# Kernel optimization log

Hardware: AMD Instinct MI355X
Metric: run time of the kernel (lower is better)

The kernel has to match this reference:

```python
import jax, jax.numpy as jnp
import numpy as np

DECAY = 0.99
EPS = 1e-05


def setup_inputs() -> dict:
    key = jax.random.key(0)
    k1, k2, k3 = jax.random.split(key, 3)
    return {
        "input": jax.random.normal(k1, (32, 64, 64, 64), dtype=jnp.float32),
        "embed": jax.random.normal(k2, (64, 512), dtype=jnp.float32),
        "cluster_size": jnp.zeros((512,), dtype=jnp.float32),
        "embed_avg": jax.random.normal(k3, (64, 512), dtype=jnp.float32),
    }


def reference(input, embed, cluster_size, embed_avg):
    n_embed = embed.shape[1]
    flatten = input.reshape(-1, input.shape[-1])  # [N, dim]
    dist = (
        jnp.sum(flatten * flatten, axis=1, keepdims=True)
        - 2.0 * flatten @ embed
        + jnp.sum(embed * embed, axis=0, keepdims=True)
    )  # [N, n_embed]
    embed_ind_flat = jnp.argmin(dist, axis=1)  # [N]
    embed_ind = embed_ind_flat.reshape(input.shape[:-1])
    quantize = jnp.take(embed.T, embed_ind_flat, axis=0).reshape(input.shape)
    diff = jnp.mean((quantize - input) ** 2)

    # EMA codebook update (training path; buffer updates returned as outputs)
    embed_onehot_sum = jnp.zeros((n_embed,), dtype=flatten.dtype).at[embed_ind_flat].add(1.0)
    embed_sum = jax.ops.segment_sum(flatten, embed_ind_flat, num_segments=n_embed).T  # [dim, n_embed]
    new_cluster_size = cluster_size * DECAY + (1.0 - DECAY) * embed_onehot_sum
    new_embed_avg = embed_avg * DECAY + (1.0 - DECAY) * embed_sum
    n = jnp.sum(new_cluster_size)
    cs = (new_cluster_size + EPS) / (n + n_embed * EPS) * n
    new_embed = new_embed_avg / cs[None, :]

    # straight-through estimator
    quantize_st = input + jax.lax.stop_gradient(quantize - input)
    return (quantize_st, diff, embed_ind, new_embed, new_cluster_size, new_embed_avg)
```

## Files before the change

kernel.cpp:

```cpp
#include <hip/hip_runtime.h>

#define DIM     64
#define N_EMBED 512
#define N_ROWS  131072
#define XPAD    132

__global__ void prep_kernel(const float* __restrict__ embed,
                            float* __restrict__ se,
                            float* __restrict__ embed_t,
                            int do_et) {
    int j = blockIdx.x * blockDim.x + threadIdx.x;
    if (j >= N_EMBED) return;
    float s = 0.f;
#pragma unroll
    for (int d = 0; d < DIM; d += 4) {
        float b0 = embed[(d + 0) * N_EMBED + j];
        float b1 = embed[(d + 1) * N_EMBED + j];
        float b2 = embed[(d + 2) * N_EMBED + j];
        float b3 = embed[(d + 3) * N_EMBED + j];
        s = fmaf(b0, b0, s); s = fmaf(b1, b1, s);
        s = fmaf(b2, b2, s); s = fmaf(b3, b3, s);
        if (do_et) {
            float4 v; v.x = b0; v.y = b1; v.z = b2; v.w = b3;
            *reinterpret_cast<float4*>(&embed_t[j * DIM + d]) = v;
        }
    }
    se[j] = s;
}

__launch_bounds__(256, 2)
__global__ void vq_assign(const float* __restrict__ input,
                          const float* __restrict__ embed,
                          const float* __restrict__ se,
                          float* __restrict__ out_ind,
                          int*   __restrict__ ind) {
    __shared__ float Xs[64][XPAD];
    __shared__ float Es[64][XPAD];
    __shared__ float sxs[128];

    const int t    = threadIdx.x;
    const int row0 = blockIdx.x * 128;
    const int tr   = t >> 4;
    const int tc   = t & 15;
    const int bx   = ((tc >> 2) & 1) * 4;

#pragma unroll
    for (int ph = 0; ph < 8; ++ph) {
        int idx = ph * 256 + t;
        int row = idx >> 4;
        int kq  = idx & 15;
        float4 v = *reinterpret_cast<const float4*>(
            &input[(size_t)(row0 + row) * 64 + kq * 4]);
        Xs[kq * 4 + 0][row] = v.x;
        Xs[kq * 4 + 1][row] = v.y;
        Xs[kq * 4 + 2][row] = v.z;
        Xs[kq * 4 + 3][row] = v.w;
    }
    __syncthreads();

    if (t < 128) {
        float s = 0.f;
#pragma unroll 8
        for (int k = 0; k < 64; ++k) { float x = Xs[k][t]; s = fmaf(x, x, s); }
        sxs[t] = s;
    }

    float bestd[8], sx[8];
    int   bestj[8];
#pragma unroll
    for (int r = 0; r < 8; ++r) { bestd[r] = INFINITY; bestj[r] = 0; }

    for (int chunk = 0; chunk < 4; ++chunk) {
        const int ccb = chunk * 128;
        __syncthreads();
#pragma unroll
        for (int ph = 0; ph < 8; ++ph) {
            int idx = ph * 256 + t;
            int k   = idx >> 5;
            int cq  = idx & 31;
            float4 v = *reinterpret_cast<const float4*>(
                &embed[k * N_EMBED + ccb + cq * 4]);
            *reinterpret_cast<float4*>(&Es[k][(cq * 4) ^ (((cq >> 3) & 1) * 4)]) = v;
        }
        __syncthreads();
        if (chunk == 0) {
#pragma unroll
            for (int r = 0; r < 8; ++r) sx[r] = sxs[tr * 8 + r];
        }

        float acc[8][8];
#pragma unroll
        for (int r = 0; r < 8; ++r)
#pragma unroll
            for (int c = 0; c < 8; ++c) acc[r][c] = 0.f;

#pragma unroll 2
        for (int k = 0; k < 64; ++k) {
            float a[8], b[8];
            *reinterpret_cast<float4*>(&a[0]) = *reinterpret_cast<const float4*>(&Xs[k][tr * 8]);
            *reinterpret_cast<float4*>(&a[4]) = *reinterpret_cast<const float4*>(&Xs[k][tr * 8 + 4]);
            *reinterpret_cast<float4*>(&b[0]) = *reinterpret_cast<const float4*>(&Es[k][(tc * 8) ^ bx]);
            *reinterpret_cast<float4*>(&b[4]) = *reinterpret_cast<const float4*>(&Es[k][(tc * 8 + 4) ^ bx]);
#pragma unroll
            for (int r = 0; r < 8; ++r)
#pragma unroll
                for (int c = 0; c < 8; ++c)
                    acc[r][c] = fmaf(a[r], b[c], acc[r][c]);
        }

#pragma unroll
        for (int c = 0; c < 8; ++c) {
            int j = ccb + tc * 8 + c;
            float sej = se[j];
#pragma unroll
            for (int r = 0; r < 8; ++r) {
                float d = (sx[r] - 2.f * acc[r][c]) + sej;
                if (d < bestd[r]) { bestd[r] = d; bestj[r] = j; }
            }
        }
    }

    __syncthreads();
    float* rd = &Es[0][0];
    int*   rj = (int*)(rd + 128 * 17);
#pragma unroll
    for (int r = 0; r < 8; ++r) {
        rd[(tr * 8 + r) * 17 + tc] = bestd[r];
        rj[(tr * 8 + r) * 17 + tc] = bestj[r];
    }
    __syncthreads();
    if (t < 128) {
        float bd = rd[t * 17 + 0];
        int   bj = rj[t * 17 + 0];
#pragma unroll
        for (int w = 1; w < 16; ++w) {
            float dw = rd[t * 17 + w];
            int   jw = rj[t * 17 + w];
            if (dw < bd || (dw == bd && jw < bj)) { bd = dw; bj = jw; }
        }
        out_ind[row0 + t] = (float)bj;
        ind[row0 + t]     = bj;
    }
}

__launch_bounds__(512, 1)
__global__ void vq_post(const float* __restrict__ input,
                        const float* __restrict__ embed,
                        const float* __restrict__ embed_t,
                        const int* __restrict__ ind,
                        float* __restrict__ out_q,
                        float* __restrict__ esum,
                        float* __restrict__ counts,
                        double* __restrict__ diff_acc,
                        int have_et) {
    __shared__ float lesum[DIM * N_EMBED];
    __shared__ float lcount[N_EMBED];
    __shared__ float wsum[8];
    const int t = threadIdx.x;

    float4* l4 = reinterpret_cast<float4*>(lesum);
#pragma unroll
    for (int i = 0; i < 16; ++i) l4[t + i * 512] = float4{0.f, 0.f, 0.f, 0.f};
    lcount[t] = 0.f;
    __syncthreads();

    const int row = blockIdx.x * 512 + t;
    const int j = ind[row];
    atomicAdd(&lcount[j], 1.0f);
    const float* rp = input + (size_t)row * DIM;
    float* oq = out_q + (size_t)row * DIM;
    float dsum = 0.f;

    if (have_et) {
        const float* qp = embed_t + (size_t)j * DIM;
#pragma unroll
        for (int d = 0; d < DIM; d += 4) {
            float4 v = *reinterpret_cast<const float4*>(rp + d);
            float4 q = *reinterpret_cast<const float4*>(qp + d);
            float t0 = q.x - v.x, t1 = q.y - v.y, t2 = q.z - v.z, t3 = q.w - v.w;
            float4 o;
            o.x = v.x + t0; o.y = v.y + t1; o.z = v.z + t2; o.w = v.w + t3;
            *reinterpret_cast<float4*>(oq + d) = o;
            dsum = fmaf(t0, t0, dsum); dsum = fmaf(t1, t1, dsum);
            dsum = fmaf(t2, t2, dsum); dsum = fmaf(t3, t3, dsum);
            atomicAdd(&lesum[(d + 0) * N_EMBED + j], v.x);
            atomicAdd(&lesum[(d + 1) * N_EMBED + j], v.y);
            atomicAdd(&lesum[(d + 2) * N_EMBED + j], v.z);
            atomicAdd(&lesum[(d + 3) * N_EMBED + j], v.w);
        }
    } else {
#pragma unroll
        for (int d = 0; d < DIM; d += 4) {
            float4 v = *reinterpret_cast<const float4*>(rp + d);
            float q0 = embed[(d + 0) * N_EMBED + j];
            float q1 = embed[(d + 1) * N_EMBED + j];
            float q2 = embed[(d + 2) * N_EMBED + j];
            float q3 = embed[(d + 3) * N_EMBED + j];
            float t0 = q0 - v.x, t1 = q1 - v.y, t2 = q2 - v.z, t3 = q3 - v.w;
            float4 o;
            o.x = v.x + t0; o.y = v.y + t1; o.z = v.z + t2; o.w = v.w + t3;
            *reinterpret_cast<float4*>(oq + d) = o;
            dsum = fmaf(t0, t0, dsum); dsum = fmaf(t1, t1, dsum);
            dsum = fmaf(t2, t2, dsum); dsum = fmaf(t3, t3, dsum);
            atomicAdd(&lesum[(d + 0) * N_EMBED + j], v.x);
            atomicAdd(&lesum[(d + 1) * N_EMBED + j], v.y);
            atomicAdd(&lesum[(d + 2) * N_EMBED + j], v.z);
            atomicAdd(&lesum[(d + 3) * N_EMBED + j], v.w);
        }
    }
    __syncthreads();

    for (int i = t; i < DIM * N_EMBED; i += 512) {
        float v = lesum[i];
        if (v != 0.f) atomicAdd(&esum[i], v);
    }
    {
        float v = lcount[t];
        if (v != 0.f) atomicAdd(&counts[t], v);
    }

    for (int off = 32; off > 0; off >>= 1) dsum += __shfl_down(dsum, off, 64);
    int lane = t & 63, wid = t >> 6;
    if (lane == 0) wsum[wid] = dsum;
    __syncthreads();
    if (t == 0) {
        float b = 0.f;
#pragma unroll
        for (int w = 0; w < 8; ++w) b += wsum[w];
        atomicAdd(diff_acc, (double)b);
    }
}

__global__ void fin_a(const float* __restrict__ cluster_size,
                      const float* __restrict__ counts,
                      float* __restrict__ out_ncs,
                      float* __restrict__ nstore) {
    int t = threadIdx.x;
    float ncs = cluster_size[t] * 0.99f + 0.01f * counts[t];
    out_ncs[t] = ncs;
    __shared__ float red[512];
    red[t] = ncs;
    __syncthreads();
    for (int s = 256; s > 0; s >>= 1) {
        if (t < s) red[t] += red[t + s];
        __syncthreads();
    }
    if (t == 0) nstore[0] = red[0];
}

__global__ void fin_b(const float* __restrict__ embed_avg,
                      const float* __restrict__ esum,
                      const float* __restrict__ out_ncs,
                      const float* __restrict__ nstore,
                      const double* __restrict__ diff_acc,
                      float* __restrict__ out_ne,
                      float* __restrict__ out_nea,
                      float* __restrict__ out_diff) {
    int e = blockIdx.x * 512 + threadIdx.x;
    const float EPSF = 1e-5f;
    float n = nstore[0];
    int j = e & (N_EMBED - 1);
    float ncs = out_ncs[j];
    float cs = (ncs + EPSF) / (n + 512.0f * EPSF) * n;
    float es = embed_avg[e] * 0.99f + 0.01f * esum[e];
    out_nea[e] = es;
    out_ne[e] = es / cs;
    if (e == 0) out_diff[0] = (float)(*diff_acc * (1.0 / 8388608.0));
}

extern "C" void kernel_launch(void* const* d_in, const int* in_sizes, int n_in,
                              void* d_out, int out_size, void* d_ws, size_t ws_size,
                              hipStream_t stream) {
    const float* input        = (const float*)d_in[0];
    const float* embed        = (const float*)d_in[1];
    const float* cluster_size = (const float*)d_in[2];
    const float* embed_avg    = (const float*)d_in[3];

    float* out_q    = (float*)d_out;
    float* out_diff = out_q + 8388608;
    float* out_ind  = out_diff + 1;
    float* out_ne   = out_ind + 131072;
    float* out_ncs  = out_ne + 32768;
    float* out_nea  = out_ncs + 512;

    char*   ws       = (char*)d_ws;
    double* diff_acc = (double*)ws;
    float*  nstore   = (float*)(ws + 64);
    float*  counts   = (float*)(ws + 256);
    float*  se       = (float*)(ws + 4096);
    int*    ind      = (int*)(ws + 8192);
    float*  esum     = (float*)(ws + 8192 + 524288);
    float*  embed_t  = (float*)(ws + 8192 + 524288 + 131072);

    const size_t need_et = 8192 + 524288 + 131072 + 131072;
    const int have_et = (ws_size >= need_et) ? 1 : 0;

    hipMemsetAsync(ws, 0, 4096, stream);
    hipMemsetAsync(ws + 8192 + 524288, 0, 131072, stream);
    prep_kernel<<<2, 256, 0, stream>>>(embed, se, embed_t, have_et);
    vq_assign<<<1024, 256, 0, stream>>>(input, embed, se, out_ind, ind);
    vq_post<<<256, 512, 0, stream>>>(input, embed, embed_t, ind, out_q, esum, counts,
                                     diff_acc, have_et);
    fin_a<<<1, 512, 0, stream>>>(cluster_size, counts, out_ncs, nstore);
    fin_b<<<64, 512, 0, stream>>>(embed_avg, esum, out_ncs, nstore, diff_acc,
                                  out_ne, out_nea, out_diff);
}
```

Before: 280.7 us.

## Replace global atomic embed-sum with per-block partials reduced in fin_b

Adds a vq_post_p kernel that accumulates per-code input sums in shared memory and writes each block's full 64x512 partial to workspace, instead of atomically merging into a global esum. fin_b then sums the partials per element, which removes global atomic contention and the esum memset. The cost is extra workspace traffic (up to 256 partial copies of 128 KB written and read back) and a serial reduction loop in fin_b. The new path is used only when the workspace is large enough; otherwise the old path runs.

Result: slower. 312.1 us (+11.2%).

```diff
diff --git a/kernel.cpp b/kernel.cpp
--- a/kernel.cpp
+++ b/kernel.cpp
@@ -140,6 +140,73 @@
         }
         out_ind[row0 + t] = (float)bj;
         ind[row0 + t]     = bj;
+    }
+}
+
+__launch_bounds__(512, 1)
+__global__ void vq_post_p(const float* __restrict__ input,
+                          const float* __restrict__ embed_t,
+                          const int* __restrict__ ind,
+                          float* __restrict__ out_q,
+                          float* __restrict__ partials,
+                          float* __restrict__ counts,
+                          double* __restrict__ diff_acc,
+                          int niter) {
+    __shared__ float lesum[DIM * N_EMBED];
+    __shared__ float lcount[N_EMBED];
+    __shared__ float wsum[8];
+    const int t = threadIdx.x;
+
+    float4* l4 = reinterpret_cast<float4*>(lesum);
+#pragma unroll
+    for (int i = 0; i < 16; ++i) l4[t + i * 512] = float4{0.f, 0.f, 0.f, 0.f};
+    lcount[t] = 0.f;
+    __syncthreads();
+
+    float dsum = 0.f;
+    for (int it = 0; it < niter; ++it) {
+        const int row = (blockIdx.x * niter + it) * 512 + t;
+        const int j = ind[row];
+        atomicAdd(&lcount[j], 1.0f);
+        const float* rp = input + (size_t)row * DIM;
+        const float* qp = embed_t + (size_t)j * DIM;
+        float* oq = out_q + (size_t)row * DIM;
+#pragma unroll
+        for (int d = 0; d < DIM; d += 4) {
+            float4 v = *reinterpret_cast<const float4*>(rp + d);
+            float4 q = *reinterpret_cast<const float4*>(qp + d);
+            float t0 = q.x - v.x, t1 = q.y - v.y, t2 = q.z - v.z, t3 = q.w - v.w;
+            float4 o;
+            o.x = v.x + t0; o.y = v.y + t1; o.z = v.z + t2; o.w = v.w + t3;
+            *reinterpret_cast<float4*>(oq + d) = o;
+            dsum = fmaf(t0, t0, dsum); dsum = fmaf(t1, t1, dsum);
+            dsum = fmaf(t2, t2, dsum); dsum = fmaf(t3, t3, dsum);
+            atomicAdd(&lesum[(d + 0) * N_EMBED + j], v.x);
+            atomicAdd(&lesum[(d + 1) * N_EMBED + j], v.y);
+            atomicAdd(&lesum[(d + 2) * N_EMBED + j], v.z);
+            atomicAdd(&lesum[(d + 3) * N_EMBED + j], v.w);
+        }
+    }
+    __syncthreads();
+
+    float* dst = partials + (size_t)blockIdx.x * (DIM * N_EMBED);
+    for (int i = t * 4; i < DIM * N_EMBED; i += 2048) {
+        *reinterpret_cast<float4*>(dst + i) = *reinterpret_cast<float4*>(&lesum[i]);
+    }
+    {
+        float v = lcount[t];
+        if (v != 0.f) atomicAdd(&counts[t], v);
+    }
+
+    for (int off = 32; off > 0; off >>= 1) dsum += __shfl_down(dsum, off, 64);
+    int lane = t & 63, wid = t >> 6;
+    if (lane == 0) wsum[wid] = dsum;
+    __syncthreads();
+    if (t == 0) {
+        float b = 0.f;
+#pragma unroll
+        for (int w = 0; w < 8; ++w) b += wsum[w];
+        atomicAdd(diff_acc, (double)b);
     }
 }
 
@@ -249,7 +316,8 @@
 }
 
 __global__ void fin_b(const float* __restrict__ embed_avg,
-                      const float* __restrict__ esum,
+                      const float* __restrict__ src,
+                      int npart,
                       const float* __restrict__ out_ncs,
                       const float* __restrict__ nstore,
                       const double* __restrict__ diff_acc,
@@ -258,11 +326,13 @@
                       float* __restrict__ out_diff) {
     int e = blockIdx.x * 512 + threadIdx.x;
     const float EPSF = 1e-5f;
+    float s = 0.f;
+    for (int p = 0; p < npart; ++p) s += src[(size_t)p * (DIM * N_EMBED) + e];
     float n = nstore[0];
     int j = e & (N_EMBED - 1);
     float ncs = out_ncs[j];
     float cs = (ncs + EPSF) / (n + 512.0f * EPSF) * n;
-    float es = embed_avg[e] * 0.99f + 0.01f * esum[e];
+    float es = embed_avg[e] * 0.99f + 0.01f * s;
     out_nea[e] = es;
     out_ne[e] = es / cs;
     if (e == 0) out_diff[0] = (float)(*diff_acc * (1.0 / 8388608.0));
@@ -291,17 +361,33 @@
     int*    ind      = (int*)(ws + 8192);
     float*  esum     = (float*)(ws + 8192 + 524288);
     float*  embed_t  = (float*)(ws + 8192 + 524288 + 131072);
-
+    float*  partials = (float*)(ws + (1 << 20));
+
+    const size_t POFF = 1 << 20;
+    int npart = 0, niter = 0;
+    if (ws_size >= POFF + (size_t)256 * 131072)      { npart = 256; niter = 1; }
+    else if (ws_size >= POFF + (size_t)64 * 131072)  { npart = 64;  niter = 4; }
     const size_t need_et = 8192 + 524288 + 131072 + 131072;
     const int have_et = (ws_size >= need_et) ? 1 : 0;
 
     hipMemsetAsync(ws, 0, 4096, stream);
-    hipMemsetAsync(ws + 8192 + 524288, 0, 131072, stream);
-    prep_kernel<<<2, 256, 0, stream>>>(embed, se, embed_t, have_et);
-    vq_assign<<<1024, 256, 0, stream>>>(input, embed, se, out_ind, ind);
-    vq_post<<<256, 512, 0, stream>>>(input, embed, embed_t, ind, out_q, esum, counts,
-                                     diff_acc, have_et);
-    fin_a<<<1, 512, 0, stream>>>(cluster_size, counts, out_ncs, nstore);
-    fin_b<<<64, 512, 0, stream>>>(embed_avg, esum, out_ncs, nstore, diff_acc,
-                                  out_ne, out_nea, out_diff);
-}
+
+    if (npart && have_et) {
+        prep_kernel<<<2, 256, 0, stream>>>(embed, se, embed_t, 1);
+        vq_assign<<<1024, 256, 0, stream>>>(input, embed, se, out_ind, ind);
+        vq_post_p<<<npart, 512, 0, stream>>>(input, embed_t, ind, out_q, partials,
+                                             counts, diff_acc, niter);
+        fin_a<<<1, 512, 0, stream>>>(cluster_size, counts, out_ncs, nstore);
+        fin_b<<<64, 512, 0, stream>>>(embed_avg, partials, npart, out_ncs, nstore,
+                                      diff_acc, out_ne, out_nea, out_diff);
+    } else {
+        hipMemsetAsync(ws + 8192 + 524288, 0, 131072, stream);
+        prep_kernel<<<2, 256, 0, stream>>>(embed, se, embed_t, have_et);
+        vq_assign<<<1024, 256, 0, stream>>>(input, embed, se, out_ind, ind);
+        vq_post<<<256, 512, 0, stream>>>(input, embed, embed_t, ind, out_q, esum,
+                                         counts, diff_acc, have_et);
+        fin_a<<<1, 512, 0, stream>>>(cluster_size, counts, out_ncs, nstore);
+        fin_b<<<64, 512, 0, stream>>>(embed_avg, esum, 1, out_ncs, nstore,
+                                      diff_acc, out_ne, out_nea, out_diff);
+    }
+}
```

## Split post pass into quantize kernel and per-code gather segment-sum kernel

Applied to the files above, without the earlier changes.

Replaces the fused post kernel, which scattered every row into a 128KB shared histogram with LDS atomics and then flushed it to global with atomics, with two kernels. The first writes the quantized output and accumulates the squared-error sum. The second gives each code its own block: the block scans the whole index array in chunks, queues the matching rows in shared memory and sums them with coalesced per-lane loads, then writes esum and counts directly with no global atomics or memset. Each of the 512 blocks rereads the full index array and the input is gathered a second time, in exchange for removing LDS atomic contention and the single-block-per-CU occupancy limit.

Result: slower. 766.3 us (+173.0%).

```diff
diff --git a/kernel.cpp b/kernel.cpp
--- a/kernel.cpp
+++ b/kernel.cpp
@@ -4,6 +4,7 @@
 #define N_EMBED 512
 #define N_ROWS  131072
 #define XPAD    132
+#define CHUNK   4096
 
 __global__ void prep_kernel(const float* __restrict__ embed,
                             float* __restrict__ se,
@@ -143,32 +144,18 @@
     }
 }
 
-__launch_bounds__(512, 1)
-__global__ void vq_post(const float* __restrict__ input,
-                        const float* __restrict__ embed,
-                        const float* __restrict__ embed_t,
-                        const int* __restrict__ ind,
-                        float* __restrict__ out_q,
-                        float* __restrict__ esum,
-                        float* __restrict__ counts,
-                        double* __restrict__ diff_acc,
-                        int have_et) {
-    __shared__ float lesum[DIM * N_EMBED];
-    __shared__ float lcount[N_EMBED];
-    __shared__ float wsum[8];
-    const int t = threadIdx.x;
-
-    float4* l4 = reinterpret_cast<float4*>(lesum);
-#pragma unroll
-    for (int i = 0; i < 16; ++i) l4[t + i * 512] = float4{0.f, 0.f, 0.f, 0.f};
-    lcount[t] = 0.f;
-    __syncthreads();
-
-    const int row = blockIdx.x * 512 + t;
-    const int j = ind[row];
-    atomicAdd(&lcount[j], 1.0f);
-    const float* rp = input + (size_t)row * DIM;
-    float* oq = out_q + (size_t)row * DIM;
+__launch_bounds__(256)
+__global__ void vq_quant(const float* __restrict__ input,
+                         const float* __restrict__ embed,
+                         const float* __restrict__ embed_t,
+                         const int* __restrict__ ind,
+                         float* __restrict__ out_q,
+                         double* __restrict__ diff_acc,
+                         int have_et) {
+    const int i = blockIdx.x * 256 + threadIdx.x;
+    const int j = ind[i];
+    const float* rp = input + (size_t)i * DIM;
+    float* oq = out_q + (size_t)i * DIM;
     float dsum = 0.f;
 
     if (have_et) {
@@ -183,10 +170,6 @@
             *reinterpret_cast<float4*>(oq + d) = o;
             dsum = fmaf(t0, t0, dsum); dsum = fmaf(t1, t1, dsum);
             dsum = fmaf(t2, t2, dsum); dsum = fmaf(t3, t3, dsum);
-            atomicAdd(&lesum[(d + 0) * N_EMBED + j], v.x);
-            atomicAdd(&lesum[(d + 1) * N_EMBED + j], v.y);
-            atomicAdd(&lesum[(d + 2) * N_EMBED + j], v.z);
-            atomicAdd(&lesum[(d + 3) * N_EMBED + j], v.w);
         }
     } else {
 #pragma unroll
@@ -202,32 +185,68 @@
             *reinterpret_cast<float4*>(oq + d) = o;
             dsum = fmaf(t0, t0, dsum); dsum = fmaf(t1, t1, dsum);
             dsum = fmaf(t2, t2, dsum); dsum = fmaf(t3, t3, dsum);
-            atomicAdd(&lesum[(d + 0) * N_EMBED + j], v.x);
-            atomicAdd(&lesum[(d + 1) * N_EMBED + j], v.y);
-            atomicAdd(&lesum[(d + 2) * N_EMBED + j], v.z);
-            atomicAdd(&lesum[(d + 3) * N_EMBED + j], v.w);
-        }
-    }
-    __syncthreads();
-
-    for (int i = t; i < DIM * N_EMBED; i += 512) {
-        float v = lesum[i];
-        if (v != 0.f) atomicAdd(&esum[i], v);
-    }
-    {
-        float v = lcount[t];
-        if (v != 0.f) atomicAdd(&counts[t], v);
+        }
     }
 
     for (int off = 32; off > 0; off >>= 1) dsum += __shfl_down(dsum, off, 64);
-    int lane = t & 63, wid = t >> 6;
+    __shared__ float wsum[4];
+    int lane = threadIdx.x & 63, wid = threadIdx.x >> 6;
     if (lane == 0) wsum[wid] = dsum;
     __syncthreads();
-    if (t == 0) {
-        float b = 0.f;
-#pragma unroll
-        for (int w = 0; w < 8; ++w) b += wsum[w];
+    if (threadIdx.x == 0) {
+        float b = wsum[0] + wsum[1] + wsum[2] + wsum[3];
         atomicAdd(diff_acc, (double)b);
+    }
+}
+
+__launch_bounds__(256, 4)
+__global__ void vq_seg(const float* __restrict__ input,
+                       const int* __restrict__ ind,
+                       float* __restrict__ esum,
+                       float* __restrict__ counts) {
+    const int j = blockIdx.x;
+    const int t = threadIdx.x;
+    const int wave = t >> 6;
+    const int lane = t & 63;
+
+    __shared__ int   queue[CHUNK];
+    __shared__ int   qn;
+    __shared__ float comb[4][64];
+
+    const int4* ind4 = reinterpret_cast<const int4*>(ind);
+    float acc = 0.f;
+    int   total = 0;
+
+    for (int base = 0; base < N_ROWS; base += CHUNK) {
+        if (t == 0) qn = 0;
+        __syncthreads();
+        const int q0 = base >> 2;
+#pragma unroll
+        for (int rep = 0; rep < CHUNK / 4 / 256; ++rep) {
+            int i4 = q0 + rep * 256 + t;
+            int4 v = ind4[i4];
+            int row = i4 * 4;
+            if (v.x == j) { int p = atomicAdd(&qn, 1); queue[p] = row; }
+            if (v.y == j) { int p = atomicAdd(&qn, 1); queue[p] = row + 1; }
+            if (v.z == j) { int p = atomicAdd(&qn, 1); queue[p] = row + 2; }
+            if (v.w == j) { int p = atomicAdd(&qn, 1); queue[p] = row + 3; }
+        }
+        __syncthreads();
+        const int n = qn;
+        total += n;
+        for (int q = wave; q < n; q += 4) {
+            int row = queue[q];
+            acc += input[(size_t)row * DIM + lane];
+        }
+        __syncthreads();
+    }
+
+    comb[wave][lane] = acc;
+    __syncthreads();
+    if (t < 64) {
+        float s = comb[0][t] + comb[1][t] + comb[2][t] + comb[3][t];
+        esum[t * N_EMBED + j] = s;
+        if (t == 0) counts[j] = (float)total;
     }
 }
 
@@ -295,12 +314,13 @@
     const size_t need_et = 8192 + 524288 + 131072 + 131072;
     const int have_et = (ws_size >= need_et) ? 1 : 0;
 
-    hipMemsetAsync(ws, 0, 4096, stream);
-    hipMemsetAsync(ws + 8192 + 524288, 0, 131072, stream);
+    hipMemsetAsync(ws, 0, 256, stream);
+
     prep_kernel<<<2, 256, 0, stream>>>(embed, se, embed_t, have_et);
     vq_assign<<<1024, 256, 0, stream>>>(input, embed, se, out_ind, ind);
-    vq_post<<<256, 512, 0, stream>>>(input, embed, embed_t, ind, out_q, esum, counts,
-                                     diff_acc, have_et);
+    vq_quant<<<512, 256, 0, stream>>>(input, embed, embed_t, ind, out_q,
+                                      diff_acc, have_et);
+    vq_seg<<<512, 256, 0, stream>>>(input, ind, esum, counts);
     fin_a<<<1, 512, 0, stream>>>(cluster_size, counts, out_ncs, nstore);
     fin_b<<<64, 512, 0, stream>>>(embed_avg, esum, out_ncs, nstore, diff_acc,
                                   out_ne, out_nea, out_diff);
```

## Restructure VQ post kernel to wave-per-row with padded LDS accumulation table

Applied to the files above, without the earlier changes.

The post-processing kernel now assigns one row per wave, with each lane handling one dimension, instead of one row per thread. Global loads and stores become fully coalesced, and LDS atomics go to a padded table (pitch 513) so the 64 lanes hit different banks rather than all contending on the same column index j. The XPAD constant also changes, which alters shared-memory padding in the assign kernel. The kernel issues more, smaller loop iterations and a per-row index broadcast load, and the padded table uses slightly more LDS.

Result: slower. 290.1 us (+3.4%).

```diff
diff --git a/kernel.cpp b/kernel.cpp
--- a/kernel.cpp
+++ b/kernel.cpp
@@ -3,7 +3,8 @@
 #define DIM     64
 #define N_EMBED 512
 #define N_ROWS  131072
-#define XPAD    132
+#define XPAD    129
+#define TPITCH  513
 
 __global__ void prep_kernel(const float* __restrict__ embed,
                             float* __restrict__ se,
@@ -144,74 +145,48 @@
 }
 
 __launch_bounds__(512, 1)
-__global__ void vq_post(const float* __restrict__ input,
-                        const float* __restrict__ embed,
-                        const float* __restrict__ embed_t,
-                        const int* __restrict__ ind,
-                        float* __restrict__ out_q,
-                        float* __restrict__ esum,
-                        float* __restrict__ counts,
-                        double* __restrict__ diff_acc,
-                        int have_et) {
-    __shared__ float lesum[DIM * N_EMBED];
+__global__ void vq_post2(const float* __restrict__ input,
+                         const float* __restrict__ embed,
+                         const float* __restrict__ embed_t,
+                         const int* __restrict__ ind,
+                         float* __restrict__ out_q,
+                         float* __restrict__ esum,
+                         float* __restrict__ counts,
+                         double* __restrict__ diff_acc,
+                         int have_et) {
+    __shared__ float tab[DIM * TPITCH];
     __shared__ float lcount[N_EMBED];
     __shared__ float wsum[8];
-    const int t = threadIdx.x;
-
-    float4* l4 = reinterpret_cast<float4*>(lesum);
-#pragma unroll
-    for (int i = 0; i < 16; ++i) l4[t + i * 512] = float4{0.f, 0.f, 0.f, 0.f};
+    const int t    = threadIdx.x;
+    const int wave = t >> 6;
+    const int lane = t & 63;
+
+    for (int i = t; i < DIM * TPITCH; i += 512) tab[i] = 0.f;
     lcount[t] = 0.f;
     __syncthreads();
 
-    const int row = blockIdx.x * 512 + t;
-    const int j = ind[row];
-    atomicAdd(&lcount[j], 1.0f);
-    const float* rp = input + (size_t)row * DIM;
-    float* oq = out_q + (size_t)row * DIM;
+    const int rbase = blockIdx.x * 512 + wave * 64;
     float dsum = 0.f;
 
-    if (have_et) {
-        const float* qp = embed_t + (size_t)j * DIM;
-#pragma unroll
-        for (int d = 0; d < DIM; d += 4) {
-            float4 v = *reinterpret_cast<const float4*>(rp + d);
-            float4 q = *reinterpret_cast<const float4*>(qp + d);
-            float t0 = q.x - v.x, t1 = q.y - v.y, t2 = q.z - v.z, t3 = q.w - v.w;
-            float4 o;
-            o.x = v.x + t0; o.y = v.y + t1; o.z = v.z + t2; o.w = v.w + t3;
-            *reinterpret_cast<float4*>(oq + d) = o;
-            dsum = fmaf(t0, t0, dsum); dsum = fmaf(t1, t1, dsum);
-            dsum = fmaf(t2, t2, dsum); dsum = fmaf(t3, t3, dsum);
-            atomicAdd(&lesum[(d + 0) * N_EMBED + j], v.x);
-            atomicAdd(&lesum[(d + 1) * N_EMBED + j], v.y);
-            atomicAdd(&lesum[(d + 2) * N_EMBED + j], v.z);
-            atomicAdd(&lesum[(d + 3) * N_EMBED + j], v.w);
-        }
-    } else {
-#pragma unroll
-        for (int d = 0; d < DIM; d += 4) {
-            float4 v = *reinterpret_cast<const float4*>(rp + d);
-            float q0 = embed[(d + 0) * N_EMBED + j];
-            float q1 = embed[(d + 1) * N_EMBED + j];
-            float q2 = embed[(d + 2) * N_EMBED + j];
-            float q3 = embed[(d + 3) * N_EMBED + j];
-            float t0 = q0 - v.x, t1 = q1 - v.y, t2 = q2 - v.z, t3 = q3 - v.w;
-            float4 o;
-            o.x = v.x + t0; o.y = v.y + t1; o.z = v.z + t2; o.w = v.w + t3;
-            *reinterpret_cast<float4*>(oq + d) = o;
-            dsum = fmaf(t0, t0, dsum); dsum = fmaf(t1, t1, dsum);
-            dsum = fmaf(t2, t2, dsum); dsum = fmaf(t3, t3, dsum);
-            atomicAdd(&lesum[(d + 0) * N_EMBED + j], v.x);
-            atomicAdd(&lesum[(d + 1) * N_EMBED + j], v.y);
-            atomicAdd(&lesum[(d + 2) * N_EMBED + j], v.z);
-            atomicAdd(&lesum[(d + 3) * N_EMBED + j], v.w);
-        }
+#pragma unroll 4
+    for (int it = 0; it < 64; ++it) {
+        const int row = rbase + it;
+        const int j = ind[row];
+        const float x = input[(size_t)row * DIM + lane];
+        float e;
+        if (have_et) e = embed_t[j * DIM + lane];
+        else         e = embed[lane * N_EMBED + j];
+        const float d0 = e - x;
+        out_q[(size_t)row * DIM + lane] = x + d0;
+        dsum = fmaf(d0, d0, dsum);
+        atomicAdd(&tab[lane * TPITCH + j], x);
+        if (lane == 0) atomicAdd(&lcount[j], 1.0f);
     }
     __syncthreads();
 
     for (int i = t; i < DIM * N_EMBED; i += 512) {
-        float v = lesum[i];
+        const int d = i >> 9, j = i & 511;
+        float v = tab[d * TPITCH + j];
         if (v != 0.f) atomicAdd(&esum[i], v);
     }
     {
@@ -220,8 +195,7 @@
     }
 
     for (int off = 32; off > 0; off >>= 1) dsum += __shfl_down(dsum, off, 64);
-    int lane = t & 63, wid = t >> 6;
-    if (lane == 0) wsum[wid] = dsum;
+    if (lane == 0) wsum[wave] = dsum;
     __syncthreads();
     if (t == 0) {
         float b = 0.f;
@@ -297,10 +271,11 @@
 
     hipMemsetAsync(ws, 0, 4096, stream);
     hipMemsetAsync(ws + 8192 + 524288, 0, 131072, stream);
+
     prep_kernel<<<2, 256, 0, stream>>>(embed, se, embed_t, have_et);
     vq_assign<<<1024, 256, 0, stream>>>(input, embed, se, out_ind, ind);
-    vq_post<<<256, 512, 0, stream>>>(input, embed, embed_t, ind, out_q, esum, counts,
-                                     diff_acc, have_et);
+    vq_post2<<<256, 512, 0, stream>>>(input, embed, embed_t, ind, out_q, esum,
+                                      counts, diff_acc, have_et);
     fin_a<<<1, 512, 0, stream>>>(cluster_size, counts, out_ncs, nstore);
     fin_b<<<64, 512, 0, stream>>>(embed_avg, esum, out_ncs, nstore, diff_acc,
                                   out_ne, out_nea, out_diff);
```
